# Kernel tuning notes

Measured on AMD Instinct MI355X. Metric: run time of the kernel, lower is better.

The kernel has to match this reference:

```python
import jax, jax.numpy as jnp
import numpy as np

# Constraint of the (buggy) original module: batch N == num_heads H == embed_size E, head_dim = 1,
# and value_len == key_len == query_len == L.
E = 64   # embed_size == num_heads == batch
H = 64
N = 64
L = 256
LN_EPS = 1e-5


def setup_inputs() -> dict:
    key = jax.random.key(0)
    ks = jax.random.split(key, 4)
    return {
        "values": jax.random.normal(ks[0], (N, L, E), dtype=jnp.float32),
        "keys": jax.random.normal(ks[1], (N, L, E), dtype=jnp.float32),
        "query": jax.random.normal(ks[2], (N, L, E), dtype=jnp.float32),
        # fc_out params (torch nn.Linear: y = x @ W.T + b)
        "W_out": jax.random.normal(ks[3], (E, E), dtype=jnp.float32) / np.float32(np.sqrt(E)),
        "b_out": jnp.zeros((E,), dtype=jnp.float32),
        # LayerNorm params
        "ln_w": jnp.ones((E,), dtype=jnp.float32),
        "ln_b": jnp.zeros((E,), dtype=jnp.float32),
    }


def reference(values, keys, query, W_out, b_out, ln_w, ln_b):
    Nb, Lq, Emb = query.shape
    Hh = H
    hd = Emb // Hh  # == 1

    def split_heads(x):
        # [N, L, E] -> [N, L, H, hd] -> permute(2,0,1,3) -> [H, N, L, hd]
        return x.reshape(Nb, -1, Hh, hd).transpose(2, 0, 1, 3)

    v = split_heads(values)   # [H, N, Lv, hd]
    k = split_heads(keys)     # [H, N, Lk, hd]
    q = split_heads(query)    # [H, N, Lq, hd]

    # torch.einsum('qnhd,knhd->qnk') on [H,N,L,hd] tensors: contract over (seq, head_dim)
    energy = jnp.einsum('anld,bnld->anb', q, k)            # [H, N, H]
    attn = jax.nn.softmax(energy / jnp.sqrt(jnp.float32(hd)), axis=-1)

    # torch.einsum('qnk,nkhd->qnhd') with values [H,N,Lv,hd]; requires N == H
    out = jnp.einsum('qnk,nkld->qnld', attn, v)            # [H, N, Lv, hd]

    # permute(1,2,0,3) -> [N, Lv, H, hd] -> view(N, Lq, E)
    out = out.transpose(1, 2, 0, 3).reshape(Nb, Lq, Emb)
    out = out @ W_out.T + b_out                            # fc_out, [N, Lq, E]

    # residual against the PERMUTED query [H,N,L,1] broadcasts to [H, N, Lq, E]
    x = out + q

    mu = jnp.mean(x, axis=-1, keepdims=True)
    var = jnp.var(x, axis=-1, keepdims=True)
    return (x - mu) / jnp.sqrt(var + LN_EPS) * ln_w + ln_b
```

## Files before the change

kernel.cpp:

```cpp
#include <hip/hip_runtime.h>
#include <stdint.h>

#define L_SEQ 256
#define E_DIM 64
#define N_B   64
#define LN_EPS 1e-5f

typedef float f4 __attribute__((ext_vector_type(4)));

__global__ __launch_bounds__(64) void attn_softmax_kernel(
    const float* __restrict__ gq,
    const float* __restrict__ gk,
    float* __restrict__ wsAttn)
{
    __shared__ float Qs[L_SEQ][16];
    __shared__ float Ks[L_SEQ][E_DIM];

    const int t  = threadIdx.x;
    const int n  = blockIdx.x >> 2;
    const int ac = blockIdx.x & 3;

    const float* qb = gq + (size_t)n * (L_SEQ * E_DIM);
    const float* kb = gk + (size_t)n * (L_SEQ * E_DIM);

    #pragma unroll 8
    for (int i = 0; i < 64; ++i) {
        int idx4 = t + 64 * i;
        int l = idx4 >> 4, c = (idx4 & 15) * 4;
        *reinterpret_cast<f4*>(&Ks[l][c]) =
            *reinterpret_cast<const f4*>(kb + (size_t)idx4 * 4);
    }
    #pragma unroll 8
    for (int i = 0; i < 16; ++i) {
        int idx4 = t + 64 * i;
        int l = idx4 >> 2, c = (idx4 & 3) * 4;
        *reinterpret_cast<f4*>(&Qs[l][c]) =
            *reinterpret_cast<const f4*>(qb + (size_t)l * E_DIM + ac * 16 + c);
    }
    __syncthreads();

    const int tx = t & 15, ty = t >> 4;
    const int b0 = tx * 4, a0 = ty * 4;

    float acc[4][4] = {};
    #pragma unroll 8
    for (int l = 0; l < L_SEQ; ++l) {
        f4 qa = *reinterpret_cast<const f4*>(&Qs[l][a0]);
        f4 kv = *reinterpret_cast<const f4*>(&Ks[l][b0]);
        #pragma unroll
        for (int ia = 0; ia < 4; ++ia)
            #pragma unroll
            for (int ib = 0; ib < 4; ++ib)
                acc[ia][ib] = fmaf(qa[ia], kv[ib], acc[ia][ib]);
    }

    #pragma unroll
    for (int ia = 0; ia < 4; ++ia) {
        float m = fmaxf(fmaxf(acc[ia][0], acc[ia][1]),
                        fmaxf(acc[ia][2], acc[ia][3]));
        #pragma unroll
        for (int s = 1; s <= 8; s <<= 1) m = fmaxf(m, __shfl_xor(m, s));
        float e0 = __expf(acc[ia][0] - m);
        float e1 = __expf(acc[ia][1] - m);
        float e2 = __expf(acc[ia][2] - m);
        float e3 = __expf(acc[ia][3] - m);
        float ssum = (e0 + e1) + (e2 + e3);
        #pragma unroll
        for (int s = 1; s <= 8; s <<= 1) ssum += __shfl_xor(ssum, s);
        float inv = 1.0f / ssum;
        acc[ia][0] = e0 * inv; acc[ia][1] = e1 * inv;
        acc[ia][2] = e2 * inv; acc[ia][3] = e3 * inv;
    }

    float* wbase = wsAttn + n * 4096 + ac * 16 + a0;
    #pragma unroll
    for (int ib = 0; ib < 4; ++ib) {
        f4 v4 = {acc[0][ib], acc[1][ib], acc[2][ib], acc[3][ib]};
        *reinterpret_cast<f4*>(wbase + (size_t)(b0 + ib) * 64) = v4;
    }
}

__global__ __launch_bounds__(256) void out_ln_kernel(
    const float* __restrict__ gv,
    const float* __restrict__ gw,
    const float* __restrict__ gbo,
    const float* __restrict__ glnw,
    const float* __restrict__ glnb,
    const float* __restrict__ wsAttn,
    float*       __restrict__ gout)
{
    __shared__ float At[64][64];
    __shared__ float Vs[64][64];
    __shared__ float Wt[64][68];
    __shared__ float Tt[64][64];

    const int t  = threadIdx.x;
    const int n  = blockIdx.x >> 2;
    const int lc = blockIdx.x & 3;
    const int l0 = lc * 64;

    const f4* asrc = reinterpret_cast<const f4*>(wsAttn + n * 4096);
    f4* adst = reinterpret_cast<f4*>(&At[0][0]);
    #pragma unroll
    for (int i = 0; i < 4; ++i) adst[t + 256 * i] = asrc[t + 256 * i];

    #pragma unroll 4
    for (int i = 0; i < 16; ++i) {
        int idx = t + 256 * i;
        int k = idx >> 6, ll = idx & 63;
        Vs[k][ll] = gv[(size_t)k * (L_SEQ * E_DIM) + (size_t)(l0 + ll) * E_DIM + n];
    }
    #pragma unroll 4
    for (int i = 0; i < 16; ++i) {
        int idx = t + 256 * i;
        int e = idx >> 6, j = idx & 63;
        Wt[j][e] = gw[idx];
    }
    __syncthreads();

    const int tx = t & 15, ty = t >> 4;

    float Ta[4][4] = {};
    #pragma unroll 8
    for (int k = 0; k < 64; ++k) {
        f4 a4 = *reinterpret_cast<const f4*>(&At[k][ty * 4]);
        f4 v4 = *reinterpret_cast<const f4*>(&Vs[k][tx * 4]);
        #pragma unroll
        for (int jj = 0; jj < 4; ++jj)
            #pragma unroll
            for (int ll = 0; ll < 4; ++ll)
                Ta[jj][ll] = fmaf(a4[jj], v4[ll], Ta[jj][ll]);
    }
    #pragma unroll
    for (int jj = 0; jj < 4; ++jj) {
        f4 w4 = {Ta[jj][0], Ta[jj][1], Ta[jj][2], Ta[jj][3]};
        *reinterpret_cast<f4*>(&Tt[ty * 4 + jj][tx * 4]) = w4;
    }
    __syncthreads();

    float fc[4][4] = {};
    #pragma unroll 8
    for (int j = 0; j < 64; ++j) {
        f4 t4 = *reinterpret_cast<const f4*>(&Tt[j][ty * 4]);
        f4 w4 = *reinterpret_cast<const f4*>(&Wt[j][tx * 4]);
        #pragma unroll
        for (int il = 0; il < 4; ++il)
            #pragma unroll
            for (int ie = 0; ie < 4; ++ie)
                fc[il][ie] = fmaf(t4[il], w4[ie], fc[il][ie]);
    }

    float be[4], lw[4], lb[4];
    #pragma unroll
    for (int ie = 0; ie < 4; ++ie) {
        be[ie] = gbo[tx * 4 + ie];
        lw[ie] = glnw[tx * 4 + ie];
        lb[ie] = glnb[tx * 4 + ie];
    }

    f4 o4[4];
    #pragma unroll
    for (int il = 0; il < 4; ++il) {
        float v0 = fc[il][0] + be[0];
        float v1 = fc[il][1] + be[1];
        float v2 = fc[il][2] + be[2];
        float v3 = fc[il][3] + be[3];
        float s1 = (v0 + v1) + (v2 + v3);
        float s2 = (v0 * v0 + v1 * v1) + (v2 * v2 + v3 * v3);
        #pragma unroll
        for (int s = 1; s <= 8; s <<= 1) {
            s1 += __shfl_xor(s1, s);
            s2 += __shfl_xor(s2, s);
        }
        float mu  = s1 * (1.0f / 64.0f);
        float var = s2 * (1.0f / 64.0f) - mu * mu;
        float rs  = rsqrtf(var + LN_EPS);
        o4[il][0] = (v0 - mu) * rs * lw[0] + lb[0];
        o4[il][1] = (v1 - mu) * rs * lw[1] + lb[1];
        o4[il][2] = (v2 - mu) * rs * lw[2] + lb[2];
        o4[il][3] = (v3 - mu) * rs * lw[3] + lb[3];
    }

    const size_t slice = (size_t)N_B * L_SEQ * E_DIM;
    float* obase = gout + (size_t)n * (L_SEQ * E_DIM)
                        + (size_t)(l0 + ty * 4) * E_DIM + tx * 4;
    #pragma unroll 4
    for (int h = 0; h < 64; ++h) {
        float* op = obase + (size_t)h * slice;
        #pragma unroll
        for (int il = 0; il < 4; ++il)
            __builtin_nontemporal_store(
                o4[il], reinterpret_cast<f4*>(op + (size_t)il * E_DIM));
    }
}

extern "C" void kernel_launch(void* const* d_in, const int* in_sizes, int n_in,
                              void* d_out, int out_size, void* d_ws, size_t ws_size,
                              hipStream_t stream)
{
    const float* gv  = (const float*)d_in[0];
    const float* gk  = (const float*)d_in[1];
    const float* gq  = (const float*)d_in[2];
    const float* gw  = (const float*)d_in[3];
    const float* gbo = (const float*)d_in[4];
    const float* glw = (const float*)d_in[5];
    const float* glb = (const float*)d_in[6];
    float* wsAttn = (float*)d_ws;
    float* out    = (float*)d_out;

    hipLaunchKernelGGL(attn_softmax_kernel, dim3(256), dim3(64), 0, stream,
                       gq, gk, wsAttn);
    hipLaunchKernelGGL(out_ln_kernel, dim3(256), dim3(256), 0, stream,
                       gv, gw, gbo, glw, glb, wsAttn, out);
}
```

Measured before the change: 307.1 us.

## Repartition attention and output kernels by batch and sequence position

The attention kernel now runs one 256-thread block per batch that loads the full Q and K tiles, instead of four 64-thread blocks that each reload K. The output kernel is reorganised so each block handles one sequence position across all batches. This makes the V load coalesced instead of a strided gather, and the attention weights are read straight from global workspace. In exchange, each block's output writes become 256-byte chunks spread across batches rather than contiguous runs, which may hurt write efficiency on the dominant output traffic.

```diff
diff --git a/kernel.cpp b/kernel.cpp
--- a/kernel.cpp
+++ b/kernel.cpp
@@ -8,34 +8,25 @@
 
 typedef float f4 __attribute__((ext_vector_type(4)));
 
-__global__ __launch_bounds__(64) void attn_softmax_kernel(
+__global__ __launch_bounds__(256) void attn_softmax_kernel(
     const float* __restrict__ gq,
     const float* __restrict__ gk,
-    float* __restrict__ wsAttn)
+    float* __restrict__ ws)
 {
-    __shared__ float Qs[L_SEQ][16];
-    __shared__ float Ks[L_SEQ][E_DIM];
-
-    const int t  = threadIdx.x;
-    const int n  = blockIdx.x >> 2;
-    const int ac = blockIdx.x & 3;
-
+    __shared__ float Qs[L_SEQ * E_DIM];
+    __shared__ float Ks[L_SEQ * E_DIM];
+
+    const int t = threadIdx.x;
+    const int n = blockIdx.x;
     const float* qb = gq + (size_t)n * (L_SEQ * E_DIM);
     const float* kb = gk + (size_t)n * (L_SEQ * E_DIM);
 
-    #pragma unroll 8
-    for (int i = 0; i < 64; ++i) {
-        int idx4 = t + 64 * i;
-        int l = idx4 >> 4, c = (idx4 & 15) * 4;
-        *reinterpret_cast<f4*>(&Ks[l][c]) =
-            *reinterpret_cast<const f4*>(kb + (size_t)idx4 * 4);
-    }
-    #pragma unroll 8
+    #pragma unroll
     for (int i = 0; i < 16; ++i) {
-        int idx4 = t + 64 * i;
-        int l = idx4 >> 2, c = (idx4 & 3) * 4;
-        *reinterpret_cast<f4*>(&Qs[l][c]) =
-            *reinterpret_cast<const f4*>(qb + (size_t)l * E_DIM + ac * 16 + c);
+        reinterpret_cast<f4*>(Qs)[t + 256 * i] =
+            reinterpret_cast<const f4*>(qb)[t + 256 * i];
+        reinterpret_cast<f4*>(Ks)[t + 256 * i] =
+            reinterpret_cast<const f4*>(kb)[t + 256 * i];
     }
     __syncthreads();
 
@@ -45,8 +36,8 @@
     float acc[4][4] = {};
     #pragma unroll 8
     for (int l = 0; l < L_SEQ; ++l) {
-        f4 qa = *reinterpret_cast<const f4*>(&Qs[l][a0]);
-        f4 kv = *reinterpret_cast<const f4*>(&Ks[l][b0]);
+        f4 qa = *reinterpret_cast<const f4*>(&Qs[l * E_DIM + a0]);
+        f4 kv = *reinterpret_cast<const f4*>(&Ks[l * E_DIM + b0]);
         #pragma unroll
         for (int ia = 0; ia < 4; ++ia)
             #pragma unroll
@@ -72,7 +63,7 @@
         acc[ia][2] = e2 * inv; acc[ia][3] = e3 * inv;
     }
 
-    float* wbase = wsAttn + n * 4096 + ac * 16 + a0;
+    float* wbase = ws + n * 4096 + a0;
     #pragma unroll
     for (int ib = 0; ib < 4; ++ib) {
         f4 v4 = {acc[0][ib], acc[1][ib], acc[2][ib], acc[3][ib]};
@@ -86,85 +77,90 @@
     const float* __restrict__ gbo,
     const float* __restrict__ glnw,
     const float* __restrict__ glnb,
-    const float* __restrict__ wsAttn,
+    const float* __restrict__ ws,
     float*       __restrict__ gout)
 {
-    __shared__ float At[64][64];
-    __shared__ float Vs[64][64];
-    __shared__ float Wt[64][68];
-    __shared__ float Tt[64][64];
-
-    const int t  = threadIdx.x;
-    const int n  = blockIdx.x >> 2;
-    const int lc = blockIdx.x & 3;
-    const int l0 = lc * 64;
-
-    const f4* asrc = reinterpret_cast<const f4*>(wsAttn + n * 4096);
-    f4* adst = reinterpret_cast<f4*>(&At[0][0]);
-    #pragma unroll
-    for (int i = 0; i < 4; ++i) adst[t + 256 * i] = asrc[t + 256 * i];
-
-    #pragma unroll 4
-    for (int i = 0; i < 16; ++i) {
-        int idx = t + 256 * i;
-        int k = idx >> 6, ll = idx & 63;
-        Vs[k][ll] = gv[(size_t)k * (L_SEQ * E_DIM) + (size_t)(l0 + ll) * E_DIM + n];
-    }
-    #pragma unroll 4
+    __shared__ float Vl[E_DIM * N_B];
+    __shared__ float Wt[64 * 68];
+    __shared__ float Tt[64 * 64];
+
+    const int t = threadIdx.x;
+    const int l = blockIdx.x;
+
+    #pragma unroll
+    for (int i = 0; i < 4; ++i) {
+        int idx4 = t + 256 * i;
+        int k = idx4 >> 4, c = (idx4 & 15) * 4;
+        reinterpret_cast<f4*>(Vl)[idx4] =
+            *reinterpret_cast<const f4*>(gv + (size_t)k * (L_SEQ * E_DIM)
+                                            + (size_t)l * E_DIM + c);
+    }
+    #pragma unroll
     for (int i = 0; i < 16; ++i) {
         int idx = t + 256 * i;
         int e = idx >> 6, j = idx & 63;
-        Wt[j][e] = gw[idx];
+        Wt[j * 68 + e] = gw[idx];
     }
     __syncthreads();
 
-    const int tx = t & 15, ty = t >> 4;
-
-    float Ta[4][4] = {};
-    #pragma unroll 8
+    const int tx = t & 15, tg = t >> 4;
+    const int j0 = tx * 4;
+    const int n0 = tg * 4;
+
+    float T[4][4] = {};
+    #pragma unroll 4
     for (int k = 0; k < 64; ++k) {
-        f4 a4 = *reinterpret_cast<const f4*>(&At[k][ty * 4]);
-        f4 v4 = *reinterpret_cast<const f4*>(&Vs[k][tx * 4]);
-        #pragma unroll
-        for (int jj = 0; jj < 4; ++jj)
+        f4 vk = *reinterpret_cast<const f4*>(&Vl[k * 64 + n0]);
+        #pragma unroll
+        for (int in = 0; in < 4; ++in) {
+            f4 a4 = *reinterpret_cast<const f4*>(
+                ws + (size_t)(n0 + in) * 4096 + k * 64 + j0);
             #pragma unroll
-            for (int ll = 0; ll < 4; ++ll)
-                Ta[jj][ll] = fmaf(a4[jj], v4[ll], Ta[jj][ll]);
-    }
-    #pragma unroll
-    for (int jj = 0; jj < 4; ++jj) {
-        f4 w4 = {Ta[jj][0], Ta[jj][1], Ta[jj][2], Ta[jj][3]};
-        *reinterpret_cast<f4*>(&Tt[ty * 4 + jj][tx * 4]) = w4;
+            for (int jj = 0; jj < 4; ++jj)
+                T[in][jj] = fmaf(a4[jj], vk[in], T[in][jj]);
+        }
+    }
+    #pragma unroll
+    for (int in = 0; in < 4; ++in) {
+        f4 w4 = {T[in][0], T[in][1], T[in][2], T[in][3]};
+        *reinterpret_cast<f4*>(&Tt[(n0 + in) * 64 + j0]) = w4;
     }
     __syncthreads();
 
+    const int e0 = tx * 4;
     float fc[4][4] = {};
-    #pragma unroll 8
-    for (int j = 0; j < 64; ++j) {
-        f4 t4 = *reinterpret_cast<const f4*>(&Tt[j][ty * 4]);
-        f4 w4 = *reinterpret_cast<const f4*>(&Wt[j][tx * 4]);
-        #pragma unroll
-        for (int il = 0; il < 4; ++il)
+    #pragma unroll 4
+    for (int jj = 0; jj < 64; jj += 4) {
+        f4 t4[4];
+        #pragma unroll
+        for (int in = 0; in < 4; ++in)
+            t4[in] = *reinterpret_cast<const f4*>(&Tt[(n0 + in) * 64 + jj]);
+        #pragma unroll
+        for (int m = 0; m < 4; ++m) {
+            f4 w4 = *reinterpret_cast<const f4*>(&Wt[(jj + m) * 68 + e0]);
             #pragma unroll
-            for (int ie = 0; ie < 4; ++ie)
-                fc[il][ie] = fmaf(t4[il], w4[ie], fc[il][ie]);
+            for (int in = 0; in < 4; ++in)
+                #pragma unroll
+                for (int ie = 0; ie < 4; ++ie)
+                    fc[in][ie] = fmaf(t4[in][m], w4[ie], fc[in][ie]);
+        }
     }
 
     float be[4], lw[4], lb[4];
     #pragma unroll
     for (int ie = 0; ie < 4; ++ie) {
-        be[ie] = gbo[tx * 4 + ie];
-        lw[ie] = glnw[tx * 4 + ie];
-        lb[ie] = glnb[tx * 4 + ie];
+        be[ie] = gbo[e0 + ie];
+        lw[ie] = glnw[e0 + ie];
+        lb[ie] = glnb[e0 + ie];
     }
 
     f4 o4[4];
     #pragma unroll
-    for (int il = 0; il < 4; ++il) {
-        float v0 = fc[il][0] + be[0];
-        float v1 = fc[il][1] + be[1];
-        float v2 = fc[il][2] + be[2];
-        float v3 = fc[il][3] + be[3];
+    for (int in = 0; in < 4; ++in) {
+        float v0 = fc[in][0] + be[0];
+        float v1 = fc[in][1] + be[1];
+        float v2 = fc[in][2] + be[2];
+        float v3 = fc[in][3] + be[3];
         float s1 = (v0 + v1) + (v2 + v3);
         float s2 = (v0 * v0 + v1 * v1) + (v2 * v2 + v3 * v3);
         #pragma unroll
@@ -175,22 +171,21 @@
         float mu  = s1 * (1.0f / 64.0f);
         float var = s2 * (1.0f / 64.0f) - mu * mu;
         float rs  = rsqrtf(var + LN_EPS);
-        o4[il][0] = (v0 - mu) * rs * lw[0] + lb[0];
-        o4[il][1] = (v1 - mu) * rs * lw[1] + lb[1];
-        o4[il][2] = (v2 - mu) * rs * lw[2] + lb[2];
-        o4[il][3] = (v3 - mu) * rs * lw[3] + lb[3];
-    }
-
-    const size_t slice = (size_t)N_B * L_SEQ * E_DIM;
-    float* obase = gout + (size_t)n * (L_SEQ * E_DIM)
-                        + (size_t)(l0 + ty * 4) * E_DIM + tx * 4;
-    #pragma unroll 4
+        o4[in][0] = (v0 - mu) * rs * lw[0] + lb[0];
+        o4[in][1] = (v1 - mu) * rs * lw[1] + lb[1];
+        o4[in][2] = (v2 - mu) * rs * lw[2] + lb[2];
+        o4[in][3] = (v3 - mu) * rs * lw[3] + lb[3];
+    }
+
+    const size_t hstride = (size_t)N_B * L_SEQ * E_DIM;
+    float* ob0 = gout + (size_t)n0 * (L_SEQ * E_DIM) + (size_t)l * E_DIM + e0;
+    #pragma unroll 8
     for (int h = 0; h < 64; ++h) {
-        float* op = obase + (size_t)h * slice;
-        #pragma unroll
-        for (int il = 0; il < 4; ++il)
+        float* op = ob0 + (size_t)h * hstride;
+        #pragma unroll
+        for (int in = 0; in < 4; ++in)
             __builtin_nontemporal_store(
-                o4[il], reinterpret_cast<f4*>(op + (size_t)il * E_DIM));
+                o4[in], reinterpret_cast<f4*>(op + (size_t)in * (L_SEQ * E_DIM)));
     }
 }
 
@@ -208,7 +203,7 @@
     float* wsAttn = (float*)d_ws;
     float* out    = (float*)d_out;
 
-    hipLaunchKernelGGL(attn_softmax_kernel, dim3(256), dim3(64), 0, stream,
+    hipLaunchKernelGGL(attn_softmax_kernel, dim3(64), dim3(256), 0, stream,
                        gq, gk, wsAttn);
     hipLaunchKernelGGL(out_ln_kernel, dim3(256), dim3(256), 0, stream,
                        gv, gw, gbo, glw, glb, wsAttn, out);
```

Result: no change. 306.0 us (-0.3%).
